# Kernel tuning notes

Hardware: AMD Instinct MI355X
Metric: run time of the kernel (lower is better)

Reference implementation:

```python
import jax, jax.numpy as jnp
import numpy as np

HEAD_DIM = 256
V_DIM = 256
HIDDEN = 1024
SCALE_BASE = 512
GAMMA = 0.96875
BATCH, SEQ = 4, 4096


def _dup_interleave(m):
    # (L, d/2) -> (L, d), duplicating each column consecutively
    return jnp.repeat(m, 2, axis=-1)


def _rotate_every_two(x):
    x1 = x[..., ::2]
    x2 = x[..., 1::2]
    return jnp.stack([-x2, x1], axis=-1).reshape(x.shape)


def _xpos(x, downscale=False):
    # x: (B, L, head_dim); offset=0 path of XPOS.forward
    B, L, Dh = x.shape
    half = Dh // 2
    scale_buf = (jnp.arange(0, Dh, 2, dtype=jnp.float32) + 0.4 * Dh) / (1.4 * Dh)  # (half,)
    pos = jnpp = jnp.arange(L, dtype=jnp.float32)
    scale = scale_buf[None, :] ** (pos / SCALE_BASE)[:, None]  # (L, half)
    inv_freq = 1.0 / (10000.0 ** (jnp.arange(half, dtype=jnp.float32) / half))
    sinusoid = pos[:, None] * inv_freq[None, :]  # (L, half)
    sin, cos = jnp.sin(sinusoid), jnp.cos(sinusoid)
    if downscale:
        scale = 1.0 / scale
    cos_s = _dup_interleave(cos * scale)  # (L, Dh)
    sin_s = _dup_interleave(sin * scale)
    return x * cos_s[None] + _rotate_every_two(x) * sin_s[None]


def _decay_matrix(L):
    n = jnp.arange(L)[:, None]
    m = jnp.arange(L)[None, :]
    mask = n >= m
    expo = jnp.where(mask, n - m, 0).astype(jnp.float32)
    return jnp.where(mask, GAMMA ** expo, 0.0)  # (L, L)


def setup_inputs() -> dict:
    key = jax.random.key(0)
    k1, k2, k3, k4 = jax.random.split(key, 4)
    X = jax.random.normal(k1, (BATCH, SEQ, HIDDEN), dtype=jnp.float32)
    W_Q = jax.random.normal(k2, (HIDDEN, HEAD_DIM), dtype=jnp.float32) / HIDDEN
    W_K = jax.random.normal(k3, (HIDDEN, HEAD_DIM), dtype=jnp.float32) / HIDDEN
    W_V = jax.random.normal(k4, (HIDDEN, V_DIM), dtype=jnp.float32) / HIDDEN
    return {"X": X, "W_Q": W_Q, "W_K": W_K, "W_V": W_V}


def reference(X, W_Q, W_K, W_V):
    L = X.shape[1]
    Q = _xpos(X @ W_Q)                      # (B, L, Dh)
    K = _xpos(X @ W_K, downscale=True)      # (B, L, Dh)
    V = X @ W_V                             # (B, L, Dv)
    D = _decay_matrix(L)                    # (L, L)
    ret = jnp.einsum('bqd,bkd->bqk', Q, K) * D[None]  # (B, L, L)
    return ret @ V                          # (B, L, Dv)
```

## Files before the change

### kernel.cpp

```cpp
#include <hip/hip_runtime.h>
#include <hip/hip_bf16.h>
#include <cstdint>
#include <cstddef>

#define L_SEQ 4096
#define BATCH_N 4
#define HID 1024
#define DH 256
#define LOG2_GAMMA (-0.045803689613124953f)
#define INV_GAMMA32 (2.7620582f)

typedef __attribute__((ext_vector_type(8))) short short8;
typedef __attribute__((ext_vector_type(4))) float floatx4;

__device__ __forceinline__ unsigned short f2bf(float f) {
    union { float f; unsigned int u; } v; v.f = f;
    unsigned int r = (v.u + 0x7FFFu + ((v.u >> 16) & 1u)) >> 16;
    return (unsigned short)r;
}

__device__ __forceinline__ void async_copy16(const unsigned short* gsrc,
                                             unsigned short* lds) {
    __builtin_amdgcn_global_load_lds(
        (const __attribute__((address_space(1))) unsigned int*)gsrc,
        (__attribute__((address_space(3))) unsigned int*)lds, 16, 0, 0);
}

__global__ __launch_bounds__(256) void prep_kernel(
    const float* __restrict__ X, unsigned short* __restrict__ Xb,
    float2* __restrict__ tabQ, float2* __restrict__ tabK,
    const float* __restrict__ WQ, const float* __restrict__ WK,
    const float* __restrict__ WV, unsigned short* __restrict__ Wt)
{
    __shared__ float Ts[64][68];
    const int bid = blockIdx.x;
    const int t   = threadIdx.x;

    if (bid < 16384) {
        const int i = (bid * 256 + t) * 4;
        const float4 v = *(const float4*)&X[i];
        ushort4 p;
        p.x = f2bf(v.x); p.y = f2bf(v.y); p.z = f2bf(v.z); p.w = f2bf(v.w);
        *(ushort4*)&Xb[i] = p;
    } else if (bid < 18432) {
        const int gid = (bid - 16384) * 256 + t;
        const int i2  = gid >> 12;
        const int pos = gid & (L_SEQ - 1);
        const float e   = (float)pos * (1.0f / 512.0f);
        const float sb  = ((float)(2 * i2) + 102.4f) * (1.0f / 358.4f);
        const float scQ = exp2f(log2f(sb) * e);
        const float scK = 1.0f / scQ;
        const float invf = exp2f(-13.287712379549449f *
                                 ((float)i2 * (1.0f / 128.0f)));
        float s, c;
        sincosf((float)pos * invf, &s, &c);
        tabQ[gid] = make_float2(c * scQ, s * scQ);
        tabK[gid] = make_float2(c * scK, s * scK);
    } else {
        const int idx = bid - 18432;
        const int n0 = (idx % 12) * 64;
        const int k0 = (idx / 12) * 64;
        const int seg = n0 >> 8;
        const float* __restrict__ W = (seg == 0) ? WQ : (seg == 1) ? WK : WV;
        const int nl0 = n0 & 255;

        const int r  = t >> 4;
        const int c4 = (t & 15) * 4;
        #pragma unroll
        for (int i = 0; i < 4; ++i) {
            const int kk = r + i * 16;
            const float4 v = *(const float4*)&W[(size_t)(k0 + kk) * DH + nl0 + c4];
            Ts[c4 + 0][kk] = v.x;
            Ts[c4 + 1][kk] = v.y;
            Ts[c4 + 2][kk] = v.z;
            Ts[c4 + 3][kk] = v.w;
        }
        __syncthreads();
        const int rn = t >> 3;
        const int c8 = (t & 7) * 8;
        #pragma unroll
        for (int i = 0; i < 2; ++i) {
            const int rr = rn + i * 32;
            ushort4 p0, p1;
            p0.x = f2bf(Ts[rr][c8 + 0]); p0.y = f2bf(Ts[rr][c8 + 1]);
            p0.z = f2bf(Ts[rr][c8 + 2]); p0.w = f2bf(Ts[rr][c8 + 3]);
            p1.x = f2bf(Ts[rr][c8 + 4]); p1.y = f2bf(Ts[rr][c8 + 5]);
            p1.z = f2bf(Ts[rr][c8 + 6]); p1.w = f2bf(Ts[rr][c8 + 7]);
            unsigned short* dst = &Wt[(size_t)(n0 + rr) * HID + k0 + c8];
            *(ushort4*)dst       = p0;
            *(ushort4*)(dst + 4) = p1;
        }
    }
}

__global__ __launch_bounds__(256) void gemm_qkv_kernel(
    const unsigned short* __restrict__ Wt,
    const unsigned short* __restrict__ Xb,
    const float2* __restrict__ tabQ,
    const float2* __restrict__ tabK,
    unsigned short* __restrict__ Qo,
    unsigned short* __restrict__ Ko,
    unsigned short* __restrict__ VtG)
{
    __shared__ unsigned short Wa[2][128][64];
    __shared__ unsigned short Xs[2][128][64];

    const int dblk = blockIdx.x;
    const int xcd  = dblk & 7;
    const int sq   = dblk >> 3;
    const int by   = xcd * 16 + sq / 6;
    const int bx   = sq % 6;

    const int n0 = bx * 128;
    const int p0 = by * 128;
    const int t    = threadIdx.x;
    const int w    = t >> 6;
    const int lane = t & 63;
    const int quad = lane >> 4;
    const int l16  = lane & 15;
    const int wn   = (w & 1) * 64;
    const int wp   = (w >> 1) * 64;

    floatx4 acc[4][4];
    #pragma unroll
    for (int i = 0; i < 4; ++i)
        #pragma unroll
        for (int j = 0; j < 4; ++j) acc[i][j] = (floatx4){0.f, 0.f, 0.f, 0.f};

    const int NT = HID / 64;

    const int g8 = lane >> 3;
    const int pc = lane & 7;
    const int sc = (pc ^ g8) * 8;
    auto stage = [&](int buf, int kt) {
        const int k0 = kt * 64;
        #pragma unroll
        for (int is = 0; is < 4; ++is) {
            const int gr = w * 8 + is * 32 + g8;
            const unsigned short* ga =
                &Wt[(size_t)(n0 + gr) * HID + k0 + sc];
            const unsigned short* gb =
                &Xb[(size_t)(p0 + gr) * HID + k0 + sc];
            async_copy16(ga, &Wa[buf][is * 32 + w * 8][0]);
            async_copy16(gb, &Xs[buf][is * 32 + w * 8][0]);
        }
    };

    stage(0, 0);
    stage(1, 1);

    const int xr = l16 & 7;

    for (int kt = 0; kt < NT; ++kt) {
        const int buf = kt & 1;
        if (kt + 1 < NT)
            asm volatile("s_waitcnt vmcnt(8)" ::: "memory");
        else
            asm volatile("s_waitcnt vmcnt(0)" ::: "memory");
        __builtin_amdgcn_s_barrier();

        const char* wbp = (const char*)&Wa[buf][0][0];
        const char* xbp = (const char*)&Xs[buf][0][0];
        short8 af[2][4], bfv[2][4];
        #pragma unroll
        for (int kk = 0; kk < 2; ++kk) {
            const int pk = (((kk << 2) | quad) ^ xr) << 4;
            #pragma unroll
            for (int nt = 0; nt < 4; ++nt) {
                af[kk][nt]  = *(const short8*)(wbp + (wn + nt * 16 + l16) * 128 + pk);
                bfv[kk][nt] = *(const short8*)(xbp + (wp + nt * 16 + l16) * 128 + pk);
            }
        }
        asm volatile("s_waitcnt lgkmcnt(0)" ::: "memory");
        __builtin_amdgcn_s_barrier();

        if (kt + 2 < NT) stage(buf, kt + 2);

        #pragma unroll
        for (int kk = 0; kk < 2; ++kk)
            #pragma unroll
            for (int nt = 0; nt < 4; ++nt)
                #pragma unroll
                for (int pt = 0; pt < 4; ++pt)
                    acc[nt][pt] = __builtin_amdgcn_mfma_f32_16x16x32_bf16(
                        af[kk][nt], bfv[kk][pt], acc[nt][pt], 0, 0, 0);
    }

    const int seg = n0 >> 8;
    const float2* __restrict__ tab = (seg == 1) ? tabK : tabQ;
    #pragma unroll
    for (int nt = 0; nt < 4; ++nt) {
        const int nfeat = n0 + wn + nt * 16 + quad * 4;
        const int d0 = nfeat & 255;
        #pragma unroll
        for (int pt = 0; pt < 4; ++pt) {
            const int pg  = p0 + wp + pt * 16 + l16;
            const int b   = pg >> 12;
            const int pos = pg & (L_SEQ - 1);
            if (seg == 2) {
                #pragma unroll
                for (int g = 0; g < 4; ++g)
                    VtG[(((size_t)(b * 256 + d0 + g)) << 12) + pos] =
                        f2bf(acc[nt][pt][g]);
            } else {
                float res[4];
                #pragma unroll
                for (int h = 0; h < 4; h += 2) {
                    const int i2 = (d0 + h) >> 1;
                    const float2 tc = tab[(i2 << 12) + pos];
                    const float cs = tc.x, ss = tc.y;
                    const float xe = acc[nt][pt][h], xo = acc[nt][pt][h + 1];
                    res[h]     = xe * cs - xo * ss;
                    res[h + 1] = xo * cs + xe * ss;
                }
                ushort4 pk;
                pk.x = f2bf(res[0]); pk.y = f2bf(res[1]);
                pk.z = f2bf(res[2]); pk.w = f2bf(res[3]);
                unsigned short* orow =
                    ((seg == 0) ? Qo : Ko) + (size_t)pg * DH + d0;
                *(ushort4*)orow = pk;
            }
        }
    }
}

__global__ __launch_bounds__(256) void retention_kernel(
    const unsigned short* __restrict__ Q,
    const unsigned short* __restrict__ K,
    const unsigned short* __restrict__ VtG,
    float* __restrict__ O)
{
    __shared__ short Ks[32][264];
    __shared__ short Vt[128][40];

    const int dblk = blockIdx.x;
    const int xcd  = dblk & 7;
    const int sq   = dblk >> 3;
    const int qt   = xcd * 8 + (sq & 7);
    const int b    = (sq >> 3) & 3;
    const int z    = sq >> 5;

    const int t  = threadIdx.x;
    const int q0 = qt * 64;

    const int w    = t >> 6;
    const int lane = t & 63;
    const int quad = lane >> 4;
    const int l16  = lane & 15;
    const int w16  = w * 16;

    const size_t rbase = (size_t)b * L_SEQ * DH;
    const size_t vbase = ((size_t)b * DH) << 12;

    int kst = q0 - 512; if (kst < 0) kst = 0;
    const int kfin = q0 + 64;

    short8 qf[8];
    {
        const unsigned short* qsrc = Q + rbase + (size_t)(q0 + w16 + l16) * DH;
        #pragma unroll
        for (int dd = 0; dd < 8; ++dd)
            qf[dd] = *(const short8*)&qsrc[dd * 32 + quad * 8];
    }

    int   dint[8];
    float dec[8];
    #pragma unroll
    for (int nt = 0; nt < 2; ++nt)
        #pragma unroll
        for (int g = 0; g < 4; ++g) {
            const int idx = nt * 4 + g;
            dint[idx] = (q0 + w16 + l16) - (kst + nt * 16 + quad * 4 + g);
            dec[idx]  = exp2f((float)dint[idx] * LOG2_GAMMA);
        }

    floatx4 o[8];
    #pragma unroll
    for (int f = 0; f < 8; ++f) o[f] = (floatx4){0.f, 0.f, 0.f, 0.f};

    const int s0   = (quad & 1) * 2;
    const int idxA = (s0 * 16 + l16) * 4;
    const int idxB = idxA + 64;
    const bool lo  = (quad < 2);

    for (int k0 = kst; k0 < kfin; k0 += 32) {
        __syncthreads();
        {
            const unsigned short* src = K + rbase + (size_t)k0 * DH;
            #pragma unroll
            for (int i = 0; i < 4; ++i) {
                const int row = i * 8 + (t >> 5);
                const int col = (t & 31) * 8;
                *(uint4*)&Ks[row][col] = *(const uint4*)&src[row * DH + col];
            }
        }
        {
            const int c0   = t >> 2;
            const int koff = (t & 3) * 8;
            #pragma unroll
            for (int i = 0; i < 2; ++i) {
                const int c = c0 + 64 * i;
                *(uint4*)&Vt[c][koff] =
                    *(const uint4*)&VtG[vbase + ((size_t)(z * 128 + c) << 12) +
                                        k0 + koff];
            }
        }
        __syncthreads();

        floatx4 sA0 = (floatx4){0.f, 0.f, 0.f, 0.f};
        floatx4 sA1 = (floatx4){0.f, 0.f, 0.f, 0.f};
        floatx4 sB0 = (floatx4){0.f, 0.f, 0.f, 0.f};
        floatx4 sB1 = (floatx4){0.f, 0.f, 0.f, 0.f};
        #pragma unroll
        for (int dd = 0; dd < 4; ++dd) {
            const short8 k0f = *(const short8*)&Ks[l16][dd * 32 + quad * 8];
            const short8 k1f = *(const short8*)&Ks[16 + l16][dd * 32 + quad * 8];
            const short8 k0g = *(const short8*)&Ks[l16][(dd + 4) * 32 + quad * 8];
            const short8 k1g = *(const short8*)&Ks[16 + l16][(dd + 4) * 32 + quad * 8];
            sA0 = __builtin_amdgcn_mfma_f32_16x16x32_bf16(k0f, qf[dd], sA0, 0, 0, 0);
            sA1 = __builtin_amdgcn_mfma_f32_16x16x32_bf16(k1f, qf[dd], sA1, 0, 0, 0);
            sB0 = __builtin_amdgcn_mfma_f32_16x16x32_bf16(k0g, qf[dd + 4], sB0, 0, 0, 0);
            sB1 = __builtin_amdgcn_mfma_f32_16x16x32_bf16(k1g, qf[dd + 4], sB1, 0, 0, 0);
        }
        const floatx4 sv0 = sA0 + sB0;
        const floatx4 sv1 = sA1 + sB1;

        unsigned int pk01[2], pk23[2];
        #pragma unroll
        for (int nt = 0; nt < 2; ++nt) {
            const floatx4 sv = nt ? sv1 : sv0;
            float pv[4];
            #pragma unroll
            for (int g = 0; g < 4; ++g) {
                const int idx = nt * 4 + g;
                pv[g] = (dint[idx] >= 0) ? sv[g] * dec[idx] : 0.0f;
            }
            pk01[nt] = ((unsigned int)f2bf(pv[1]) << 16) | (unsigned int)f2bf(pv[0]);
            pk23[nt] = ((unsigned int)f2bf(pv[3]) << 16) | (unsigned int)f2bf(pv[2]);
        }
        #pragma unroll
        for (int i = 0; i < 8; ++i) { dint[i] -= 32; dec[i] *= INV_GAMMA32; }

        const int a01_0 = __builtin_amdgcn_ds_bpermute(idxA, (int)pk01[0]);
        const int a01_1 = __builtin_amdgcn_ds_bpermute(idxA, (int)pk01[1]);
        const int a23_0 = __builtin_amdgcn_ds_bpermute(idxA, (int)pk23[0]);
        const int a23_1 = __builtin_amdgcn_ds_bpermute(idxA, (int)pk23[1]);
        const int b01_0 = __builtin_amdgcn_ds_bpermute(idxB, (int)pk01[0]);
        const int b01_1 = __builtin_amdgcn_ds_bpermute(idxB, (int)pk01[1]);
        const int b23_0 = __builtin_amdgcn_ds_bpermute(idxB, (int)pk23[0]);
        const int b23_1 = __builtin_amdgcn_ds_bpermute(idxB, (int)pk23[1]);
        union { int u[4]; short8 s8; } af;
        af.u[0] = lo ? a01_0 : a01_1;
        af.u[1] = lo ? a23_0 : a23_1;
        af.u[2] = lo ? b01_0 : b01_1;
        af.u[3] = lo ? b23_0 : b23_1;

        #pragma unroll
        for (int f = 0; f < 8; ++f) {
            const short8 bfr = *(const short8*)&Vt[f * 16 + l16][quad * 8];
            o[f] = __builtin_amdgcn_mfma_f32_16x16x32_bf16(af.s8, bfr, o[f], 0, 0, 0);
        }
    }

    #pragma unroll
    for (int f = 0; f < 8; ++f) {
        #pragma unroll
        for (int g = 0; g < 4; ++g) {
            const int qpos = q0 + w16 + quad * 4 + g;
            O[rbase + (size_t)qpos * DH + z * 128 + f * 16 + l16] = o[f][g];
        }
    }
}

extern "C" void kernel_launch(void* const* d_in, const int* in_sizes, int n_in,
                              void* d_out, int out_size, void* d_ws, size_t ws_size,
                              hipStream_t stream)
{
    const float* X  = (const float*)d_in[0];
    const float* WQ = (const float*)d_in[1];
    const float* WK = (const float*)d_in[2];
    const float* WV = (const float*)d_in[3];
    float* out = (float*)d_out;

    const size_t per = (size_t)BATCH_N * L_SEQ * DH;
    unsigned short* Qw  = (unsigned short*)d_ws;
    unsigned short* Kw  = Qw + per;
    unsigned short* Vtw = Kw + per;
    unsigned short* Xbw = Vtw + per;
    unsigned short* Wtw = Xbw + (size_t)16384 * HID;
    float2* tabQ = (float2*)(Wtw + 786432);
    float2* tabK = tabQ + (size_t)128 * L_SEQ;

    prep_kernel<<<18624, 256, 0, stream>>>(X, Xbw, tabQ, tabK,
                                           WQ, WK, WV, Wtw);

    gemm_qkv_kernel<<<768, 256, 0, stream>>>(Wtw, Xbw, tabQ, tabK, Qw, Kw, Vtw);

    retention_kernel<<<512, 256, 0, stream>>>(Qw, Kw, Vtw, out);
}
```

Baseline: 203.0 us.

## Double-buffer K/V tiles via async global-to-LDS loads with XOR swizzle

Replaces the synchronous register-staged K and V tile loads with async global_load_lds copies into double-buffered LDS, prefetching the next tile while the current one is computed. The padded layouts become unpadded and XOR-swizzled to avoid bank conflicts, and s_setprio is raised around MFMA sections. This is meant to hide global load latency and cut one barrier per iteration. In exchange it doubles LDS use, which may lower occupancy, and depends on the swizzle matching the direct-to-LDS write pattern.

New measurement: 187.7 us. 1.08x faster.

```diff
diff --git a/kernel.cpp b/kernel.cpp
--- a/kernel.cpp
+++ b/kernel.cpp
@@ -230,8 +230,8 @@
     const unsigned short* __restrict__ VtG,
     float* __restrict__ O)
 {
-    __shared__ short Ks[32][264];
-    __shared__ short Vt[128][40];
+    __shared__ unsigned short Ks[2][32][256];
+    __shared__ unsigned short Vt[2][128][32];
 
     const int dblk = blockIdx.x;
     const int xcd  = dblk & 7;
@@ -253,7 +253,25 @@
     const size_t vbase = ((size_t)b * DH) << 12;
 
     int kst = q0 - 512; if (kst < 0) kst = 0;
-    const int kfin = q0 + 64;
+    const int nsteps = ((q0 + 64) - kst) >> 5;
+
+    const int krow = w * 2 + (lane >> 5);
+    const int kscol = ((lane & 31) ^ (krow & 7)) * 8;
+    const int vrow = w * 16 + (lane >> 2);
+    const int vscol = ((lane & 3) ^ ((lane >> 3) & 3)) * 8;
+
+    auto stage = [&](int buf, int k0) {
+        const unsigned short* ksrc = K + rbase + (size_t)k0 * DH;
+        #pragma unroll
+        for (int i = 0; i < 4; ++i)
+            async_copy16(&ksrc[(size_t)(i * 8 + krow) * DH + kscol],
+                         &Ks[buf][i * 8 + w * 2][0]);
+        #pragma unroll
+        for (int i = 0; i < 2; ++i)
+            async_copy16(&VtG[vbase + ((size_t)(z * 128 + i * 64 + vrow) << 12) +
+                              k0 + vscol],
+                         &Vt[buf][i * 64 + w * 16][0]);
+    };
 
     short8 qf[8];
     {
@@ -283,45 +301,40 @@
     const int idxB = idxA + 64;
     const bool lo  = (quad < 2);
 
-    for (int k0 = kst; k0 < kfin; k0 += 32) {
-        __syncthreads();
-        {
-            const unsigned short* src = K + rbase + (size_t)k0 * DH;
-            #pragma unroll
-            for (int i = 0; i < 4; ++i) {
-                const int row = i * 8 + (t >> 5);
-                const int col = (t & 31) * 8;
-                *(uint4*)&Ks[row][col] = *(const uint4*)&src[row * DH + col];
-            }
-        }
-        {
-            const int c0   = t >> 2;
-            const int koff = (t & 3) * 8;
-            #pragma unroll
-            for (int i = 0; i < 2; ++i) {
-                const int c = c0 + 64 * i;
-                *(uint4*)&Vt[c][koff] =
-                    *(const uint4*)&VtG[vbase + ((size_t)(z * 128 + c) << 12) +
-                                        k0 + koff];
-            }
-        }
-        __syncthreads();
+    const int xk7 = l16 & 7;
+    const int pvx = (quad ^ ((l16 >> 1) & 3)) << 4;
+
+    stage(0, kst);
+    asm volatile("s_waitcnt vmcnt(0)" ::: "memory");
+    __builtin_amdgcn_s_barrier();
+
+    for (int it = 0; it < nsteps; ++it) {
+        const int cur = it & 1;
+        const int k0  = kst + it * 32;
+        if (it + 1 < nsteps) stage(cur ^ 1, k0 + 32);
+
+        const char* kb = (const char*)&Ks[cur][0][0];
+        const char* vb = (const char*)&Vt[cur][0][0];
 
         floatx4 sA0 = (floatx4){0.f, 0.f, 0.f, 0.f};
         floatx4 sA1 = (floatx4){0.f, 0.f, 0.f, 0.f};
         floatx4 sB0 = (floatx4){0.f, 0.f, 0.f, 0.f};
         floatx4 sB1 = (floatx4){0.f, 0.f, 0.f, 0.f};
+        __builtin_amdgcn_s_setprio(1);
         #pragma unroll
         for (int dd = 0; dd < 4; ++dd) {
-            const short8 k0f = *(const short8*)&Ks[l16][dd * 32 + quad * 8];
-            const short8 k1f = *(const short8*)&Ks[16 + l16][dd * 32 + quad * 8];
-            const short8 k0g = *(const short8*)&Ks[l16][(dd + 4) * 32 + quad * 8];
-            const short8 k1g = *(const short8*)&Ks[16 + l16][(dd + 4) * 32 + quad * 8];
+            const int c0 = ((dd * 4 + quad) ^ xk7) << 4;
+            const int c1 = (((dd + 4) * 4 + quad) ^ xk7) << 4;
+            const short8 k0f = *(const short8*)(kb + l16 * 512 + c0);
+            const short8 k1f = *(const short8*)(kb + (16 + l16) * 512 + c0);
+            const short8 k0g = *(const short8*)(kb + l16 * 512 + c1);
+            const short8 k1g = *(const short8*)(kb + (16 + l16) * 512 + c1);
             sA0 = __builtin_amdgcn_mfma_f32_16x16x32_bf16(k0f, qf[dd], sA0, 0, 0, 0);
             sA1 = __builtin_amdgcn_mfma_f32_16x16x32_bf16(k1f, qf[dd], sA1, 0, 0, 0);
             sB0 = __builtin_amdgcn_mfma_f32_16x16x32_bf16(k0g, qf[dd + 4], sB0, 0, 0, 0);
             sB1 = __builtin_amdgcn_mfma_f32_16x16x32_bf16(k1g, qf[dd + 4], sB1, 0, 0, 0);
         }
+        __builtin_amdgcn_s_setprio(0);
         const floatx4 sv0 = sA0 + sB0;
         const floatx4 sv1 = sA1 + sB1;
 
@@ -355,11 +368,17 @@
         af.u[2] = lo ? b01_0 : b01_1;
         af.u[3] = lo ? b23_0 : b23_1;
 
+        __builtin_amdgcn_s_setprio(1);
         #pragma unroll
         for (int f = 0; f < 8; ++f) {
-            const short8 bfr = *(const short8*)&Vt[f * 16 + l16][quad * 8];
+            const short8 bfr =
+                *(const short8*)(vb + (f * 16 + l16) * 64 + pvx);
             o[f] = __builtin_amdgcn_mfma_f32_16x16x32_bf16(af.s8, bfr, o[f], 0, 0, 0);
         }
+        __builtin_amdgcn_s_setprio(0);
+
+        asm volatile("s_waitcnt vmcnt(0)" ::: "memory");
+        __builtin_amdgcn_s_barrier();
     }
 
     #pragma unroll
```
